# Kernel optimization log

Hardware: AMD Instinct MI355X
Metric: run time of the kernel (lower is better)

The kernel has to match this reference:

```python
import jax, jax.numpy as jnp
import numpy as np

B, J, N = 64, 32, 4096
Q_DIM, K_DIM, V_DIM, H = 130, 128, 130, 4


def _init_linear(key, fan_in, fan_out):
    kw, kb = jax.random.split(key)
    bound = 1.0 / np.sqrt(fan_in)
    W = jax.random.uniform(kw, (fan_in, fan_out), jnp.float32, -bound, bound)
    b = jax.random.uniform(kb, (fan_out,), jnp.float32, -bound, bound)
    return W, b


def setup_inputs() -> dict:
    key = jax.random.key(0)
    ks = jax.random.split(key, 10)
    joint_q = jax.random.normal(ks[0], (B, J, Q_DIM), jnp.float32)
    vertex_k = jax.random.normal(ks[1], (B, N, K_DIM), jnp.float32)
    vertex_v = jax.random.normal(ks[2], (B, N, V_DIM), jnp.float32)
    vertex_mask = jax.random.bernoulli(ks[3], 0.1, (B, N))  # True = masked
    # joint_q_encoder: Linear(130,64) ReLU Linear(64, 128*4)
    W1, b1 = _init_linear(ks[4], Q_DIM, 64)
    W2, b2 = _init_linear(ks[5], 64, K_DIM * H)
    # joint_output_layer: Linear(520,64) ReLU Linear(64,32) ReLU Linear(32,1)
    W3, b3 = _init_linear(ks[6], V_DIM * H, 64)
    W4, b4 = _init_linear(ks[7], 64, 32)
    W5, b5 = _init_linear(ks[8], 32, 1)
    return {
        "joint_q": joint_q, "vertex_k": vertex_k, "vertex_v": vertex_v,
        "vertex_mask": vertex_mask,
        "W1": W1, "b1": b1, "W2": W2, "b2": b2,
        "W3": W3, "b3": b3, "W4": W4, "b4": b4, "W5": W5, "b5": b5,
    }


def reference(joint_q, vertex_k, vertex_v, vertex_mask,
              W1, b1, W2, b2, W3, b3, W4, b4, W5, b5):
    b, j, _ = joint_q.shape
    # Encode queries: [B,J,130] -> [B,J,H,K]
    h = jax.nn.relu(joint_q @ W1 + b1)
    q = (h @ W2 + b2).reshape(b, j, H, K_DIM)
    # Attention scores via broadcasted contraction (avoids materializing
    # the expanded K/V copies the torch code builds): [B,J,H,N]
    scores = jnp.einsum('bjhk,bnk->bjhn', q, vertex_k) / np.sqrt(K_DIM).astype(np.float32)
    scores = jnp.where(vertex_mask[:, None, None, :], jnp.float32(-1e9), scores)
    attn = jax.nn.softmax(scores, axis=-1)
    # Weighted values: [B,J,H,V] -> [B,J,H*V]
    out = jnp.einsum('bjhn,bnv->bjhv', attn, vertex_v).reshape(b, j, H * V_DIM)
    # Output MLP -> [B,J]
    out = jax.nn.relu(out @ W3 + b3)
    out = jax.nn.relu(out @ W4 + b4)
    out = (out @ W5 + b5).squeeze(-1)
    return out
```

## Files before the change

kernel.cpp:

```cpp
#include <hip/hip_runtime.h>
#include <hip/hip_bf16.h>

#define BB 64
#define JJ 32
#define NN 4096
#define QD 130
#define KD 128
#define VD 130
#define HH 4
#define CT 8
#define NCH (NN / CT)
#define TIL (NCH / 32)
#define PSTRIDE (JJ + JJ + JJ * VD)

typedef __attribute__((ext_vector_type(8))) __bf16 bf16x8;
typedef __attribute__((ext_vector_type(4))) float  f32x4;

union FW4 { unsigned int u[4]; bf16x8 v; };

#define SEL_HI 0x07060302u

__device__ __forceinline__ unsigned int packhi(float f0, float f1) {
    return __builtin_amdgcn_perm(__float_as_uint(f1), __float_as_uint(f0), SEL_HI);
}
__device__ __forceinline__ float truncbf(float f) {
    return __uint_as_float(__float_as_uint(f) & 0xFFFF0000u);
}
__device__ __forceinline__ void split8(float4 a, float4 b, bf16x8* h, bf16x8* l) {
    FW4 H, L;
    H.u[0] = packhi(a.x, a.y);
    H.u[1] = packhi(a.z, a.w);
    H.u[2] = packhi(b.x, b.y);
    H.u[3] = packhi(b.z, b.w);
    L.u[0] = packhi(a.x - truncbf(a.x), a.y - truncbf(a.y));
    L.u[1] = packhi(a.z - truncbf(a.z), a.w - truncbf(a.w));
    L.u[2] = packhi(b.x - truncbf(b.x), b.y - truncbf(b.y));
    L.u[3] = packhi(b.z - truncbf(b.z), b.w - truncbf(b.w));
    *h = H.v; *l = L.v;
}

__global__ __launch_bounds__(64) void enc_kernel(
        const float* __restrict__ jq,
        const float* __restrict__ W1, const float* __restrict__ b1,
        const float* __restrict__ W2, const float* __restrict__ b2,
        float* __restrict__ qenc) {
    int row = blockIdx.x;
    int t = threadIdx.x;
    __shared__ float x[QD];
    __shared__ float h[64];
    for (int i = t; i < QD; i += 64) x[i] = jq[row * QD + i];
    __syncthreads();
    float a0 = 0.f, a1 = 0.f;
    for (int i = 0; i < QD - 1; i += 2) {
        a0 += x[i] * W1[i * 64 + t];
        a1 += x[i + 1] * W1[(i + 1) * 64 + t];
    }
    h[t] = fmaxf(b1[t] + a0 + a1, 0.f);
    __syncthreads();
    float a[8];
    #pragma unroll
    for (int s = 0; s < 8; ++s) a[s] = b2[t + 64 * s];
    for (int i = 0; i < 64; ++i) {
        float hv = h[i];
        #pragma unroll
        for (int s = 0; s < 8; ++s) a[s] += hv * W2[i * 512 + t + 64 * s];
    }
    #pragma unroll
    for (int s = 0; s < 8; ++s) qenc[row * 512 + t + 64 * s] = a[s];
}

__global__ __launch_bounds__(512, 2) void attn_kernel(
        const float* __restrict__ Kg, const float* __restrict__ Vg,
        const int* __restrict__ maskg, const float* __restrict__ qenc,
        float* __restrict__ part) {
    int blk = blockIdx.x;
    int c = blk & (CT - 1);
    int b = blk / CT;
    int tid = threadIdx.x;
    int wid = tid >> 6;
    int lane = tid & 63;
    int h = wid & 3;
    int qhalf = wid >> 2;
    int g = lane >> 4;
    int q15 = lane & 15;

    __shared__ __align__(16) __bf16 Kf[2][2][2][4][65][8];
    __shared__ __align__(16) __bf16 Vf[2][2][8][64][8];
    __shared__ float Vt_s[2][2][32];
    __shared__ int   msks[2][32];

    int skey = tid >> 4;
    int sdhi = tid & 15;
    int sa = skey >> 3, sb = skey & 7;
    int skh = sb >> 2;
    int sm  = skh ? 4 * (sa ^ 2) + (sb & 3)
                  : 4 * sa + sb;
    int slK = sm + 16 * (sdhi & 3);
    int skst = sdhi >> 2;
    int sv = tid & 127, skb = tid >> 7;
    int svc = sv >> 4;
    int slV = (sv & 15) + 16 * skb;

    const float* Kb = Kg + (size_t)b * NN * KD;
    const float* Vb = Vg + (size_t)b * NN * VD;
    const int*   Mb = maskg + b * NN;

    float4 kfa, kfb;
    float  vf[8];
    float2 vt = {0.f, 0.f};
    int    mk = 0;

    auto sload = [&](int T) {
        int n0 = c * NCH + T * 32;
        const float* ks = Kb + (size_t)(n0 + skey) * KD + sdhi * 8;
        kfa = *(const float4*)ks;
        kfb = *(const float4*)(ks + 4);
        const float* vs = Vb + (size_t)(n0 + skb * 8) * VD + sv;
        #pragma unroll
        for (int j = 0; j < 8; ++j) vf[j] = vs[(size_t)j * VD];
        if (tid < 32) {
            vt = *(const float2*)(Vb + (size_t)(n0 + tid) * VD + 128);
            mk = Mb[n0 + tid];
        }
    };
    auto swrite = [&](int buf) {
        bf16x8 hh, ll;
        split8(kfa, kfb, &hh, &ll);
        *(bf16x8*)&Kf[buf][0][skh][skst][slK][0] = hh;
        *(bf16x8*)&Kf[buf][1][skh][skst][slK][0] = ll;
        float4 va = {vf[0], vf[1], vf[2], vf[3]};
        float4 vb2 = {vf[4], vf[5], vf[6], vf[7]};
        split8(va, vb2, &hh, &ll);
        *(bf16x8*)&Vf[buf][0][svc][slV][0] = hh;
        *(bf16x8*)&Vf[buf][1][svc][slV][0] = ll;
        if (tid < 32) {
            Vt_s[buf][0][tid] = vt.x;
            Vt_s[buf][1][tid] = vt.y;
            msks[buf][tid] = mk;
        }
    };

    sload(0);

    bf16x8 qh[4], ql[4];
    {
        const float* qrow = qenc + (size_t)(b * JJ + qhalf * 16 + q15) * 512
                            + h * KD + g * 8;
        #pragma unroll
        for (int kst = 0; kst < 4; ++kst) {
            float4 qa = *(const float4*)(qrow + kst * 32);
            float4 qb = *(const float4*)(qrow + kst * 32 + 4);
            split8(qa, qb, &qh[kst], &ql[kst]);
        }
    }

    swrite(0);
    sload(1);
    __builtin_amdgcn_sched_barrier(0);

    f32x4 O[8];
    #pragma unroll
    for (int vc = 0; vc < 8; ++vc)
        #pragma unroll
        for (int r = 0; r < 4; ++r) O[vc][r] = 0.f;
    float acct0 = 0.f, acct1 = 0.f;
    float m_run = -1e30f, l_run = 0.f;

    __syncthreads();

    for (int t = 0; t < TIL; ++t) {
        int cur = t & 1;

        if (t + 1 < TIL) {
            swrite(cur ^ 1);
            int T2 = (t + 2 < TIL) ? (t + 2) : t;
            sload(T2);
        }
        __builtin_amdgcn_sched_barrier(0);

        unsigned int mword = (unsigned int)__ballot(msks[cur][lane & 31] != 0);

        f32x4 S[2];
        #pragma unroll
        for (int kh = 0; kh < 2; ++kh)
            #pragma unroll
            for (int r = 0; r < 4; ++r) S[kh][r] = 0.f;
        #pragma unroll
        for (int kst = 0; kst < 4; ++kst) {
            #pragma unroll
            for (int kh = 0; kh < 2; ++kh) {
                bf16x8 khf = *(const bf16x8*)&Kf[cur][0][kh][kst][lane][0];
                bf16x8 klf = *(const bf16x8*)&Kf[cur][1][kh][kst][lane][0];
                S[kh] = __builtin_amdgcn_mfma_f32_16x16x32_bf16(khf, qh[kst], S[kh], 0, 0, 0);
                S[kh] = __builtin_amdgcn_mfma_f32_16x16x32_bf16(khf, ql[kst], S[kh], 0, 0, 0);
                S[kh] = __builtin_amdgcn_mfma_f32_16x16x32_bf16(klf, qh[kst], S[kh], 0, 0, 0);
            }
        }

        const float sc = 0.08838834764831845f;
        float sp[8];
        float rm = -1e30f;
        #pragma unroll
        for (int r = 0; r < 4; ++r) {
            int key0 = 8 * g + r;
            float s0 = ((mword >> key0) & 1u) ? -1e30f : S[0][r] * sc;
            sp[r] = s0;
            rm = fmaxf(rm, s0);
            int key1 = 8 * (g ^ 2) + 4 + r;
            float s1 = ((mword >> key1) & 1u) ? -1e30f : S[1][r] * sc;
            sp[4 + r] = s1;
            rm = fmaxf(rm, s1);
        }
        rm = fmaxf(rm, __shfl_xor(rm, 16));
        rm = fmaxf(rm, __shfl_xor(rm, 32));
        if (!__all(rm <= m_run + 8.f)) {
            float mn = fmaxf(m_run, rm);
            float rs = __expf(m_run - mn);
            m_run = mn;
            l_run *= rs; acct0 *= rs; acct1 *= rs;
            #pragma unroll
            for (int r = 0; r < 4; ++r) {
                float rr = __shfl(rs, g * 4 + r);
                #pragma unroll
                for (int vc = 0; vc < 8; ++vc) O[vc][r] *= rr;
            }
        }
        float ps = 0.f;
        #pragma unroll
        for (int i = 0; i < 8; ++i) {
            float p = __expf(sp[i] - m_run);
            sp[i] = p;
            ps += p;
        }
        ps += __shfl_xor(ps, 16);
        ps += __shfl_xor(ps, 32);
        l_run += ps;

        #pragma unroll
        for (int r = 0; r < 4; ++r) {
            int key0 = 8 * g + r;
            int key1 = 8 * (g ^ 2) + 4 + r;
            acct0 += sp[r] * Vt_s[cur][0][key0] + sp[4 + r] * Vt_s[cur][0][key1];
            acct1 += sp[r] * Vt_s[cur][1][key0] + sp[4 + r] * Vt_s[cur][1][key1];
        }

        unsigned w0h = packhi(sp[0], sp[1]), w1h = packhi(sp[2], sp[3]);
        unsigned w2h = packhi(sp[4], sp[5]), w3h = packhi(sp[6], sp[7]);
        unsigned w0l = packhi(sp[0] - truncbf(sp[0]), sp[1] - truncbf(sp[1]));
        unsigned w1l = packhi(sp[2] - truncbf(sp[2]), sp[3] - truncbf(sp[3]));
        unsigned w2l = packhi(sp[4] - truncbf(sp[4]), sp[5] - truncbf(sp[5]));
        unsigned w3l = packhi(sp[6] - truncbf(sp[6]), sp[7] - truncbf(sp[7]));
        FW4 PH, PL;
        PH.u[0] = w0h; PH.u[1] = w1h;
        PH.u[2] = __shfl_xor(w2h, 32);
        PH.u[3] = __shfl_xor(w3h, 32);
        PL.u[0] = w0l; PL.u[1] = w1l;
        PL.u[2] = __shfl_xor(w2l, 32);
        PL.u[3] = __shfl_xor(w3l, 32);
        bf16x8 PAH = PH.v, PAL = PL.v;

        #pragma unroll
        for (int vc = 0; vc < 8; ++vc) {
            bf16x8 vh = *(const bf16x8*)&Vf[cur][0][vc][lane][0];
            bf16x8 vl = *(const bf16x8*)&Vf[cur][1][vc][lane][0];
            O[vc] = __builtin_amdgcn_mfma_f32_16x16x32_bf16(PAH, vh, O[vc], 0, 0, 0);
            O[vc] = __builtin_amdgcn_mfma_f32_16x16x32_bf16(PAL, vh, O[vc], 0, 0, 0);
            O[vc] = __builtin_amdgcn_mfma_f32_16x16x32_bf16(PAH, vl, O[vc], 0, 0, 0);
        }

        __syncthreads();
    }

    float* P = part + (size_t)((b * HH + h) * CT + c) * PSTRIDE;
    if (lane < 16) {
        P[qhalf * 16 + lane] = m_run;
        P[JJ + qhalf * 16 + lane] = l_run;
    }
    float* A = P + 2 * JJ;
    #pragma unroll
    for (int vc = 0; vc < 8; ++vc) {
        #pragma unroll
        for (int r = 0; r < 4; ++r) {
            int q = qhalf * 16 + g * 4 + r;
            A[q * VD + vc * 16 + q15] = O[vc][r];
        }
    }
    acct0 += __shfl_xor(acct0, 16);
    acct0 += __shfl_xor(acct0, 32);
    acct1 += __shfl_xor(acct1, 16);
    acct1 += __shfl_xor(acct1, 32);
    if (lane < 16) {
        A[(qhalf * 16 + lane) * VD + 128] = acct0;
        A[(qhalf * 16 + lane) * VD + 129] = acct1;
    }
}

__global__ __launch_bounds__(64) void comb_mlp_kernel(
        const float* __restrict__ part,
        const float* __restrict__ W3, const float* __restrict__ b3,
        const float* __restrict__ W4, const float* __restrict__ b4,
        const float* __restrict__ W5, const float* __restrict__ b5,
        float* __restrict__ out) {
    int row = blockIdx.x;
    int b = row >> 5;
    int j = row & 31;
    int t = threadIdx.x;
    __shared__ float w_s[HH][CT];
    __shared__ float x[HH * VD];
    __shared__ float h1[64];
    __shared__ float h2[32];

    if (t < HH * CT) {
        int h = t / CT, cc = t % CT;
        const float* P = part + (size_t)((b * HH + h) * CT + cc) * PSTRIDE;
        float m = P[j];
        float l = P[JJ + j];
        float mm = m;
        #pragma unroll
        for (int s = 1; s < CT; s <<= 1) mm = fmaxf(mm, __shfl_xor(mm, s));
        float e = __expf(m - mm);
        float L = l * e;
        #pragma unroll
        for (int s = 1; s < CT; s <<= 1) L += __shfl_xor(L, s);
        w_s[h][cc] = (L > 0.f) ? e / L : 0.f;
    }
    __syncthreads();

    for (int idx = t; idx < HH * VD; idx += 64) {
        int h = idx / VD, v = idx - h * VD;
        const float* A = part + (size_t)(b * HH + h) * CT * PSTRIDE + 2 * JJ + j * VD + v;
        float o = 0.f;
        #pragma unroll 4
        for (int cc = 0; cc < CT; ++cc) o += w_s[h][cc] * A[(size_t)cc * PSTRIDE];
        x[idx] = o;
    }
    __syncthreads();

    float a0 = 0.f, a1 = 0.f, a2 = 0.f, a3 = 0.f;
    for (int i = 0; i < HH * VD; i += 4) {
        a0 += x[i] * W3[i * 64 + t];
        a1 += x[i + 1] * W3[(i + 1) * 64 + t];
        a2 += x[i + 2] * W3[(i + 2) * 64 + t];
        a3 += x[i + 3] * W3[(i + 3) * 64 + t];
    }
    h1[t] = fmaxf(b3[t] + (a0 + a1) + (a2 + a3), 0.f);
    __syncthreads();
    if (t < 32) {
        float c0 = 0.f, c1 = 0.f;
        for (int i = 0; i < 64; i += 2) {
            c0 += h1[i] * W4[i * 32 + t];
            c1 += h1[i + 1] * W4[(i + 1) * 32 + t];
        }
        h2[t] = fmaxf(b4[t] + c0 + c1, 0.f);
    }
    __syncthreads();
    if (t == 0) {
        float a3f = b5[0];
        for (int i = 0; i < 32; ++i) a3f += h2[i] * W5[i];
        out[row] = a3f;
    }
}

extern "C" void kernel_launch(void* const* d_in, const int* in_sizes, int n_in,
                              void* d_out, int out_size, void* d_ws, size_t ws_size,
                              hipStream_t stream) {
    const float* jq = (const float*)d_in[0];
    const float* Kg = (const float*)d_in[1];
    const float* Vg = (const float*)d_in[2];
    const int* mask = (const int*)d_in[3];
    const float* W1 = (const float*)d_in[4];
    const float* b1 = (const float*)d_in[5];
    const float* W2 = (const float*)d_in[6];
    const float* b2 = (const float*)d_in[7];
    const float* W3 = (const float*)d_in[8];
    const float* b3 = (const float*)d_in[9];
    const float* W4 = (const float*)d_in[10];
    const float* b4 = (const float*)d_in[11];
    const float* W5 = (const float*)d_in[12];
    const float* b5 = (const float*)d_in[13];
    float* out = (float*)d_out;

    float* ws = (float*)d_ws;
    float* qenc = ws;
    float* part = qenc + (size_t)BB * JJ * HH * KD;

    enc_kernel<<<BB * JJ, 64, 0, stream>>>(jq, W1, b1, W2, b2, qenc);
    attn_kernel<<<BB * CT, 512, 0, stream>>>(Kg, Vg, mask, qenc, part);
    comb_mlp_kernel<<<BB * JJ, 64, 0, stream>>>(part, W3, b3, W4, b4, W5, b5, out);
}
```

Baseline: 119.3 us.

## Single-buffer V tile and split K/V prefetch into staged pipeline

Splits the per-tile global loads and LDS writes into separate K and V stages. K stays double-buffered and is prefetched two tiles ahead, while V, the V tail and the mask are now single-buffered and loaded one tile ahead. A mid-iteration barrier after the QK MFMAs separates the stages. This roughly halves the V-related LDS footprint and drops the K padding row, which may allow better occupancy or cache behaviour. The cost is an extra __syncthreads per tile, and the V store now sits right before the QK MFMAs on the critical path.

Measured after the change: 129.7 us. +8.8%, slower.

```diff
diff --git a/kernel.cpp b/kernel.cpp
--- a/kernel.cpp
+++ b/kernel.cpp
@@ -84,10 +84,10 @@
     int g = lane >> 4;
     int q15 = lane & 15;
 
-    __shared__ __align__(16) __bf16 Kf[2][2][2][4][65][8];
-    __shared__ __align__(16) __bf16 Vf[2][2][8][64][8];
-    __shared__ float Vt_s[2][2][32];
-    __shared__ int   msks[2][32];
+    __shared__ __align__(16) __bf16 Kf[2][2][2][4][64][8];
+    __shared__ __align__(16) __bf16 Vf[2][8][64][8];
+    __shared__ float Vt_s[2][32];
+    __shared__ int   msks[32];
 
     int skey = tid >> 4;
     int sdhi = tid & 15;
@@ -110,11 +110,14 @@
     float2 vt = {0.f, 0.f};
     int    mk = 0;
 
-    auto sload = [&](int T) {
+    auto sloadK = [&](int T) {
         int n0 = c * NCH + T * 32;
         const float* ks = Kb + (size_t)(n0 + skey) * KD + sdhi * 8;
         kfa = *(const float4*)ks;
         kfb = *(const float4*)(ks + 4);
+    };
+    auto sloadV = [&](int T) {
+        int n0 = c * NCH + T * 32;
         const float* vs = Vb + (size_t)(n0 + skb * 8) * VD + sv;
         #pragma unroll
         for (int j = 0; j < 8; ++j) vf[j] = vs[(size_t)j * VD];
@@ -123,24 +126,28 @@
             mk = Mb[n0 + tid];
         }
     };
-    auto swrite = [&](int buf) {
+    auto swriteK = [&](int buf) {
         bf16x8 hh, ll;
         split8(kfa, kfb, &hh, &ll);
         *(bf16x8*)&Kf[buf][0][skh][skst][slK][0] = hh;
         *(bf16x8*)&Kf[buf][1][skh][skst][slK][0] = ll;
+    };
+    auto swriteV = [&]() {
+        bf16x8 hh, ll;
         float4 va = {vf[0], vf[1], vf[2], vf[3]};
         float4 vb2 = {vf[4], vf[5], vf[6], vf[7]};
         split8(va, vb2, &hh, &ll);
-        *(bf16x8*)&Vf[buf][0][svc][slV][0] = hh;
-        *(bf16x8*)&Vf[buf][1][svc][slV][0] = ll;
+        *(bf16x8*)&Vf[0][svc][slV][0] = hh;
+        *(bf16x8*)&Vf[1][svc][slV][0] = ll;
         if (tid < 32) {
-            Vt_s[buf][0][tid] = vt.x;
-            Vt_s[buf][1][tid] = vt.y;
-            msks[buf][tid] = mk;
+            Vt_s[0][tid] = vt.x;
+            Vt_s[1][tid] = vt.y;
+            msks[tid] = mk;
         }
     };
 
-    sload(0);
+    sloadK(0);
+    sloadV(0);
 
     bf16x8 qh[4], ql[4];
     {
@@ -154,8 +161,8 @@
         }
     }
 
-    swrite(0);
-    sload(1);
+    swriteK(0);
+    sloadK(1);
     __builtin_amdgcn_sched_barrier(0);
 
     f32x4 O[8];
@@ -171,14 +178,9 @@
     for (int t = 0; t < TIL; ++t) {
         int cur = t & 1;
 
-        if (t + 1 < TIL) {
-            swrite(cur ^ 1);
-            int T2 = (t + 2 < TIL) ? (t + 2) : t;
-            sload(T2);
-        }
+        swriteV();
+        if (t + 1 < TIL) swriteK(cur ^ 1);
         __builtin_amdgcn_sched_barrier(0);
-
-        unsigned int mword = (unsigned int)__ballot(msks[cur][lane & 31] != 0);
 
         f32x4 S[2];
         #pragma unroll
@@ -197,6 +199,13 @@
             }
         }
 
+        __syncthreads();
+
+        if (t + 2 < TIL) sloadK(t + 2);
+        if (t + 1 < TIL) sloadV(t + 1);
+        __builtin_amdgcn_sched_barrier(0);
+
+        unsigned int mword = (unsigned int)__ballot(msks[lane & 31] != 0);
         const float sc = 0.08838834764831845f;
         float sp[8];
         float rm = -1e30f;
@@ -240,8 +249,8 @@
         for (int r = 0; r < 4; ++r) {
             int key0 = 8 * g + r;
             int key1 = 8 * (g ^ 2) + 4 + r;
-            acct0 += sp[r] * Vt_s[cur][0][key0] + sp[4 + r] * Vt_s[cur][0][key1];
-            acct1 += sp[r] * Vt_s[cur][1][key0] + sp[4 + r] * Vt_s[cur][1][key1];
+            acct0 += sp[r] * Vt_s[0][key0] + sp[4 + r] * Vt_s[0][key1];
+            acct1 += sp[r] * Vt_s[1][key0] + sp[4 + r] * Vt_s[1][key1];
         }
 
         unsigned w0h = packhi(sp[0], sp[1]), w1h = packhi(sp[2], sp[3]);
@@ -261,8 +270,8 @@
 
         #pragma unroll
         for (int vc = 0; vc < 8; ++vc) {
-            bf16x8 vh = *(const bf16x8*)&Vf[cur][0][vc][lane][0];
-            bf16x8 vl = *(const bf16x8*)&Vf[cur][1][vc][lane][0];
+            bf16x8 vh = *(const bf16x8*)&Vf[0][vc][lane][0];
+            bf16x8 vl = *(const bf16x8*)&Vf[1][vc][lane][0];
             O[vc] = __builtin_amdgcn_mfma_f32_16x16x32_bf16(PAH, vh, O[vc], 0, 0, 0);
             O[vc] = __builtin_amdgcn_mfma_f32_16x16x32_bf16(PAL, vh, O[vc], 0, 0, 0);
             O[vc] = __builtin_amdgcn_mfma_f32_16x16x32_bf16(PAH, vl, O[vc], 0, 0, 0);
```

## Software-pipeline PV MFMA across tiles, pad LDS rows, halve key chunks

Applied to the files above, without the earlier changes.

Each iteration now runs the P·V MFMAs for the previous tile right after the Q·K MFMAs of the current tile. K and V shared-memory writes are split into separate phases with extra barriers, so global loads and LDS stores overlap more compute. LDS rows are padded to a stride of 17 to reduce bank conflicts on fragment reads. The number of key chunks per batch drops from 8 to 4, which halves the grid and the partial-merge work but gives each block twice as many tiles, risking underfilled CUs.

Result: faster. 109.7 us (-8.0%).

```diff
diff --git a/kernel.cpp b/kernel.cpp
--- a/kernel.cpp
+++ b/kernel.cpp
@@ -8,7 +8,7 @@
 #define KD 128
 #define VD 130
 #define HH 4
-#define CT 8
+#define CT 4
 #define NCH (NN / CT)
 #define TIL (NCH / 32)
 #define PSTRIDE (JJ + JJ + JJ * VD)
@@ -75,7 +75,7 @@
         float* __restrict__ part) {
     int blk = blockIdx.x;
     int c = blk & (CT - 1);
-    int b = blk / CT;
+    int b = blk >> 2;
     int tid = threadIdx.x;
     int wid = tid >> 6;
     int lane = tid & 63;
@@ -83,9 +83,10 @@
     int qhalf = wid >> 2;
     int g = lane >> 4;
     int q15 = lane & 15;
-
-    __shared__ __align__(16) __bf16 Kf[2][2][2][4][65][8];
-    __shared__ __align__(16) __bf16 Vf[2][2][8][64][8];
+    int idx17 = q15 + 17 * g;
+
+    __shared__ __align__(16) __bf16 Kf[2][2][2][4][68][8];
+    __shared__ __align__(16) __bf16 Vf[2][2][8][68][8];
     __shared__ float Vt_s[2][2][32];
     __shared__ int   msks[2][32];
 
@@ -95,11 +96,10 @@
     int skh = sb >> 2;
     int sm  = skh ? 4 * (sa ^ 2) + (sb & 3)
                   : 4 * sa + sb;
-    int slK = sm + 16 * (sdhi & 3);
+    int slK = sm + 17 * (sdhi & 3);
     int skst = sdhi >> 2;
     int sv = tid & 127, skb = tid >> 7;
-    int svc = sv >> 4;
-    int slV = (sv & 15) + 16 * skb;
+    int svc = sv >> 4, slV = (sv & 15) + 17 * skb;
 
     const float* Kb = Kg + (size_t)b * NN * KD;
     const float* Vb = Vg + (size_t)b * NN * VD;
@@ -110,11 +110,14 @@
     float2 vt = {0.f, 0.f};
     int    mk = 0;
 
-    auto sload = [&](int T) {
+    auto sloadK = [&](int T) {
         int n0 = c * NCH + T * 32;
         const float* ks = Kb + (size_t)(n0 + skey) * KD + sdhi * 8;
         kfa = *(const float4*)ks;
         kfb = *(const float4*)(ks + 4);
+    };
+    auto sloadV = [&](int T) {
+        int n0 = c * NCH + T * 32;
         const float* vs = Vb + (size_t)(n0 + skb * 8) * VD + sv;
         #pragma unroll
         for (int j = 0; j < 8; ++j) vf[j] = vs[(size_t)j * VD];
@@ -123,11 +126,14 @@
             mk = Mb[n0 + tid];
         }
     };
-    auto swrite = [&](int buf) {
+    auto swriteK = [&](int buf) {
         bf16x8 hh, ll;
         split8(kfa, kfb, &hh, &ll);
         *(bf16x8*)&Kf[buf][0][skh][skst][slK][0] = hh;
         *(bf16x8*)&Kf[buf][1][skh][skst][slK][0] = ll;
+    };
+    auto swriteV = [&](int buf) {
+        bf16x8 hh, ll;
         float4 va = {vf[0], vf[1], vf[2], vf[3]};
         float4 vb2 = {vf[4], vf[5], vf[6], vf[7]};
         split8(va, vb2, &hh, &ll);
@@ -140,7 +146,8 @@
         }
     };
 
-    sload(0);
+    sloadK(0);
+    sloadV(0);
 
     bf16x8 qh[4], ql[4];
     {
@@ -154,8 +161,10 @@
         }
     }
 
-    swrite(0);
-    sload(1);
+    swriteK(0);
+    swriteV(0);
+    sloadK(1);
+    sloadV(1);
     __builtin_amdgcn_sched_barrier(0);
 
     f32x4 O[8];
@@ -165,20 +174,12 @@
         for (int r = 0; r < 4; ++r) O[vc][r] = 0.f;
     float acct0 = 0.f, acct1 = 0.f;
     float m_run = -1e30f, l_run = 0.f;
+    bf16x8 PAH = {}, PAL = {};
 
     __syncthreads();
 
     for (int t = 0; t < TIL; ++t) {
         int cur = t & 1;
-
-        if (t + 1 < TIL) {
-            swrite(cur ^ 1);
-            int T2 = (t + 2 < TIL) ? (t + 2) : t;
-            sload(T2);
-        }
-        __builtin_amdgcn_sched_barrier(0);
-
-        unsigned int mword = (unsigned int)__ballot(msks[cur][lane & 31] != 0);
 
         f32x4 S[2];
         #pragma unroll
@@ -189,14 +190,28 @@
         for (int kst = 0; kst < 4; ++kst) {
             #pragma unroll
             for (int kh = 0; kh < 2; ++kh) {
-                bf16x8 khf = *(const bf16x8*)&Kf[cur][0][kh][kst][lane][0];
-                bf16x8 klf = *(const bf16x8*)&Kf[cur][1][kh][kst][lane][0];
+                bf16x8 khf = *(const bf16x8*)&Kf[cur][0][kh][kst][idx17][0];
+                bf16x8 klf = *(const bf16x8*)&Kf[cur][1][kh][kst][idx17][0];
                 S[kh] = __builtin_amdgcn_mfma_f32_16x16x32_bf16(khf, qh[kst], S[kh], 0, 0, 0);
                 S[kh] = __builtin_amdgcn_mfma_f32_16x16x32_bf16(khf, ql[kst], S[kh], 0, 0, 0);
                 S[kh] = __builtin_amdgcn_mfma_f32_16x16x32_bf16(klf, qh[kst], S[kh], 0, 0, 0);
             }
         }
-
+        if (t > 0) {
+            #pragma unroll
+            for (int vc = 0; vc < 8; ++vc) {
+                bf16x8 vh = *(const bf16x8*)&Vf[cur ^ 1][0][vc][idx17][0];
+                bf16x8 vl = *(const bf16x8*)&Vf[cur ^ 1][1][vc][idx17][0];
+                O[vc] = __builtin_amdgcn_mfma_f32_16x16x32_bf16(PAH, vh, O[vc], 0, 0, 0);
+                O[vc] = __builtin_amdgcn_mfma_f32_16x16x32_bf16(PAL, vh, O[vc], 0, 0, 0);
+                O[vc] = __builtin_amdgcn_mfma_f32_16x16x32_bf16(PAH, vl, O[vc], 0, 0, 0);
+            }
+        }
+        __builtin_amdgcn_sched_barrier(0);
+        if (t + 1 < TIL) swriteK((t + 1) & 1);
+        __syncthreads();
+
+        unsigned int mword = (unsigned int)__ballot(msks[cur][lane & 31] != 0);
         const float sc = 0.08838834764831845f;
         float sp[8];
         float rm = -1e30f;
@@ -257,18 +272,24 @@
         PL.u[0] = w0l; PL.u[1] = w1l;
         PL.u[2] = __shfl_xor(w2l, 32);
         PL.u[3] = __shfl_xor(w3l, 32);
-        bf16x8 PAH = PH.v, PAL = PL.v;
-
+        PAH = PH.v; PAL = PL.v;
+
+        __builtin_amdgcn_sched_barrier(0);
+        if (t + 1 < TIL) swriteV((t + 1) & 1);
+        if (t + 2 < TIL) { sloadK(t + 2); sloadV(t + 2); }
+        __syncthreads();
+    }
+
+    {
+        int lastb = (TIL - 1) & 1;
         #pragma unroll
         for (int vc = 0; vc < 8; ++vc) {
-            bf16x8 vh = *(const bf16x8*)&Vf[cur][0][vc][lane][0];
-            bf16x8 vl = *(const bf16x8*)&Vf[cur][1][vc][lane][0];
+            bf16x8 vh = *(const bf16x8*)&Vf[lastb][0][vc][idx17][0];
+            bf16x8 vl = *(const bf16x8*)&Vf[lastb][1][vc][idx17][0];
             O[vc] = __builtin_amdgcn_mfma_f32_16x16x32_bf16(PAH, vh, O[vc], 0, 0, 0);
             O[vc] = __builtin_amdgcn_mfma_f32_16x16x32_bf16(PAL, vh, O[vc], 0, 0, 0);
             O[vc] = __builtin_amdgcn_mfma_f32_16x16x32_bf16(PAH, vl, O[vc], 0, 0, 0);
         }
-
-        __syncthreads();
     }
 
     float* P = part + (size_t)((b * HH + h) * CT + c) * PSTRIDE;
@@ -330,7 +351,7 @@
         int h = idx / VD, v = idx - h * VD;
         const float* A = part + (size_t)(b * HH + h) * CT * PSTRIDE + 2 * JJ + j * VD + v;
         float o = 0.f;
-        #pragma unroll 4
+        #pragma unroll
         for (int cc = 0; cc < CT; ++cc) o += w_s[h][cc] * A[(size_t)cc * PSTRIDE];
         x[idx] = o;
     }
```
